# Optimization experiments

Measured on AMD Instinct MI355X. Metric: run time of the kernel, lower is better.

Reference implementation:

```python
import jax, jax.numpy as jnp
import numpy as np

N_NODES = 100000
N_FEAT = 512
HIDDEN = 256
N_CLASSES = 40
N_EDGES = 1600000
K = 10
ALPHA = 0.1


def setup_inputs() -> dict:
    key = jax.random.key(0)
    ks = jax.random.split(key, 8)
    feat = jax.random.normal(ks[0], (N_NODES, N_FEAT), dtype=jnp.float32)
    src = jax.random.randint(ks[1], (N_EDGES,), 0, N_NODES, dtype=jnp.int32)
    dst = jax.random.randint(ks[2], (N_EDGES,), 0, N_NODES, dtype=jnp.int32)
    # linear layers (PyTorch-style uniform init)
    s1 = 1.0 / np.sqrt(N_FEAT)
    W1 = jax.random.uniform(ks[3], (N_FEAT, HIDDEN), minval=-s1, maxval=s1, dtype=jnp.float32)
    b1 = jax.random.uniform(ks[4], (HIDDEN,), minval=-s1, maxval=s1, dtype=jnp.float32)
    s2 = 1.0 / np.sqrt(HIDDEN)
    W2 = jax.random.uniform(ks[5], (HIDDEN, N_CLASSES), minval=-s2, maxval=s2, dtype=jnp.float32)
    b2 = jax.random.uniform(ks[6], (N_CLASSES,), minval=-s2, maxval=s2, dtype=jnp.float32)
    # PPR init for per-hop weights: temp[k] = alpha*(1-alpha)^k, temp[K] = (1-alpha)^K
    temp = ALPHA * (1.0 - ALPHA) ** np.arange(K + 1)
    temp[-1] = (1.0 - ALPHA) ** K
    temp = jnp.asarray(temp, dtype=jnp.float32)
    return {"feat": feat, "W1": W1, "b1": b1, "W2": W2, "b2": b2,
            "temp": temp, "src": src, "dst": dst}


def reference(feat, W1, b1, W2, b2, temp, src, dst):
    N = feat.shape[0]
    # dgl.add_self_loop
    loop = jnp.arange(N, dtype=src.dtype)
    src_f = jnp.concatenate([src, loop])
    dst_f = jnp.concatenate([dst, loop])
    # MLP: lin1 -> relu -> lin2 (dropout is identity at inference)
    h = jax.nn.relu(feat @ W1 + b1) @ W2 + b2  # [N, C]
    # symmetric normalization: norm_e = d[dst] * d[src], d = deg^{-1/2}
    deg = jax.ops.segment_sum(jnp.ones_like(dst_f, dtype=h.dtype), dst_f, num_segments=N)
    d = jax.lax.rsqrt(deg)  # deg >= 1 due to self loops
    norm = (d[dst_f] * d[src_f])[:, None]  # [E, 1]
    # K-hop propagation with learned per-hop weights
    TH = h * temp[0]
    for k in range(K):
        msg = h[src_f] * norm                     # gather + edge scale
        h = jax.ops.segment_sum(msg, dst_f, num_segments=N)  # scatter-sum
        TH = TH + h * temp[k + 1]
    return jax.nn.log_softmax(TH, axis=1)
```

## Files before the change

kernel.cpp:

```cpp
#include <hip/hip_runtime.h>
#include <math.h>
#include <stdint.h>

#define N_NODES 100000
#define N_FEAT  512
#define HIDDEN  256
#define N_CLS   40
#define N_EDGES 1600000
#define K_HOPS  10

#define NPART   8
#define PSZ     12500
#define NPN     (NPART * N_NODES)
#define SCANB   782
#define HPAD    64

#define PB      51
#define PGRID   ((N_NODES + PB - 1) / PB)
#define ECAP    2048

typedef __attribute__((ext_vector_type(8))) short short8;
typedef __attribute__((ext_vector_type(4))) float f4_t;

__device__ __forceinline__ short f2bf(float f) {
    union { float f; unsigned u; } x; x.f = f;
    unsigned r = x.u + 0x7fffu + ((x.u >> 16) & 1u);
    return (short)(r >> 16);
}

__device__ __forceinline__ float bf2f(short b) {
    union { unsigned u; float f; } x;
    x.u = ((unsigned)(unsigned short)b) << 16;
    return x.f;
}

__device__ __forceinline__ unsigned cvtpk(float lo, float hi) {
    unsigned r;
    asm("v_cvt_pk_bf16_f32 %0, %1, %2" : "=v"(r) : "v"(lo), "v"(hi));
    return r;
}


__global__ __launch_bounds__(256) void init_degp_kernel(int* __restrict__ degp) {
    int idx = blockIdx.x * 256 + threadIdx.x;
    if (idx < NPN) {
        int v = idx >> 3, p = idx & 7;
        degp[idx] = (p == v / PSZ) ? 1 : 0;
    }
}

__global__ __launch_bounds__(256) void count_dst_kernel(const int* __restrict__ src,
                                                        const int* __restrict__ dst,
                                                        int* __restrict__ degp) {
    int e = blockIdx.x * 256 + threadIdx.x;
    if (e < N_EDGES) atomicAdd(&degp[dst[e] * NPART + src[e] / PSZ], 1);
}

__global__ __launch_bounds__(256) void rsqrt_deg_kernel(const int* __restrict__ degp,
                                                        float* __restrict__ d) {
    int v = blockIdx.x * 256 + threadIdx.x;
    if (v < N_NODES) {
        int s = 0;
#pragma unroll
        for (int p = 0; p < NPART; ++p) s += degp[v * NPART + p];
        d[v] = rsqrtf((float)s);
    }
}


__global__ __launch_bounds__(1024) void scan_partial_kernel(const int* __restrict__ degp,
                                                            int* __restrict__ blocksum) {
    __shared__ int s[1024];
    int t = threadIdx.x;
    int idx = blockIdx.x * 1024 + t;
    s[t] = (idx < NPN) ? degp[idx] : 0;
    __syncthreads();
#pragma unroll
    for (int off = 512; off > 0; off >>= 1) {
        if (t < off) s[t] += s[t + off];
        __syncthreads();
    }
    if (t == 0) blocksum[blockIdx.x] = s[0];
}

__global__ __launch_bounds__(1024) void scan_blocks_kernel(const int* __restrict__ blocksum,
                                                           int* __restrict__ blockoff) {
    __shared__ int s[1024];
    int t = threadIdx.x;
    int v = (t < SCANB) ? blocksum[t] : 0;
    s[t] = v;
    __syncthreads();
#pragma unroll
    for (int off = 1; off < 1024; off <<= 1) {
        int add = (t >= off) ? s[t - off] : 0;
        __syncthreads();
        s[t] += add;
        __syncthreads();
    }
    if (t < SCANB) blockoff[t] = s[t] - v;
}

__global__ __launch_bounds__(1024) void scan_write_kernel(const int* __restrict__ degp,
                                                          const int* __restrict__ blockoff,
                                                          int* __restrict__ rowptrp,
                                                          int* __restrict__ cursor) {
    __shared__ int s[1024];
    int t = threadIdx.x;
    int idx = blockIdx.x * 1024 + t;
    int v = (idx < NPN) ? degp[idx] : 0;
    s[t] = v;
    __syncthreads();
#pragma unroll
    for (int off = 1; off < 1024; off <<= 1) {
        int add = (t >= off) ? s[t - off] : 0;
        __syncthreads();
        s[t] += add;
        __syncthreads();
    }
    int pre = s[t] - v + blockoff[blockIdx.x];
    if (idx <= NPN) rowptrp[idx] = pre;
    if (idx < NPN) cursor[idx] = pre;
}

__global__ __launch_bounds__(256) void scatter_edges_kernel(const int* __restrict__ src,
                                                            const int* __restrict__ dst,
                                                            const float* __restrict__ d,
                                                            int* __restrict__ cursor,
                                                            int2* __restrict__ epair) {
    int e = blockIdx.x * 256 + threadIdx.x;
    if (e >= N_EDGES) return;
    int u = src[e], v = dst[e];
    int pos = atomicAdd(&cursor[v * NPART + u / PSZ], 1);
    int2 p;
    p.x = u * 128;
    p.y = __float_as_int(d[u] * d[v]);
    epair[pos] = p;
}

__global__ __launch_bounds__(256) void scatter_self_kernel(const float* __restrict__ d,
                                                           int* __restrict__ cursor,
                                                           int2* __restrict__ epair) {
    int v = blockIdx.x * 256 + threadIdx.x;
    if (v >= N_NODES) return;
    int pos = atomicAdd(&cursor[v * NPART + v / PSZ], 1);
    float dv = d[v];
    int2 p;
    p.x = v * 128;
    p.y = __float_as_int(dv * dv);
    epair[pos] = p;
}

__global__ __launch_bounds__(256) void cvt_w1_kernel(const float* __restrict__ W1,
                                                     short* __restrict__ W1T) {
    int lin = blockIdx.x * 256 + threadIdx.x;
    int k = lin >> 8, n = lin & 255;
    W1T[n * 512 + k] = f2bf(W1[lin]);
}

__global__ __launch_bounds__(256) void cvt_w2_kernel(const float* __restrict__ W2,
                                                     short* __restrict__ W2T) {
    int lin = blockIdx.x * 256 + threadIdx.x;
    int n = lin >> 8, k = lin & 255;
    W2T[lin] = (n < N_CLS) ? f2bf(W2[k * N_CLS + n]) : (short)0;
}

__global__ __launch_bounds__(256) void mlp_kernel(const float* __restrict__ feat,
                                                  const short* __restrict__ W1T,
                                                  const float* __restrict__ b1,
                                                  const short* __restrict__ W2T,
                                                  const float* __restrict__ b2,
                                                  const float* __restrict__ temp,
                                                  short* __restrict__ h,
                                                  float* __restrict__ TH) {
    __shared__ union {
        short A[2][64][72];
        short sH[64][264];
        struct { short Ho[64][40]; float To[64][40]; } o;
    } S;

    const int tid = threadIdx.x;
    const int rbase = blockIdx.x * 64;
    const int lane = tid & 63;
    const int wv = tid >> 6;
    const int quad = lane >> 4;
    const int l15 = lane & 15;

    f4_t acc[4][4];
#pragma unroll
    for (int m = 0; m < 4; ++m)
#pragma unroll
        for (int n = 0; n < 4; ++n) acc[m][n] = (f4_t)0.f;

    const int srow = tid >> 2;
    const int scol = (tid & 3) * 16;
    int growc = rbase + srow;
    if (growc >= N_NODES) growc = N_NODES - 1;
    const float* fp = feat + (size_t)growc * N_FEAT + scol;

    f4_t fR0, fR1, fR2, fR3;
    short8 bR[8];

#define LOADF(KT)                                                   \
    { const f4_t* p_ = (const f4_t*)(fp + (KT) * 64);               \
      fR0 = p_[0]; fR1 = p_[1]; fR2 = p_[2]; fR3 = p_[3]; }

#define LOADB(KT)                                                   \
    { const short* wb_ = W1T + (KT) * 64;                           \
      _Pragma("unroll")                                             \
      for (int kk2 = 0; kk2 < 2; ++kk2)                             \
          _Pragma("unroll")                                         \
          for (int n = 0; n < 4; ++n)                               \
              bR[kk2 * 4 + n] = *(const short8*)(                   \
                  wb_ + (wv * 64 + n * 16 + l15) * 512 + kk2 * 32 + quad * 8); }

#define CVTWR(BUF)                                                  \
    { union { unsigned u[4]; short8 s; } xlo_, xhi_;                \
      xlo_.u[0] = cvtpk(fR0[0], fR0[1]); xlo_.u[1] = cvtpk(fR0[2], fR0[3]); \
      xlo_.u[2] = cvtpk(fR1[0], fR1[1]); xlo_.u[3] = cvtpk(fR1[2], fR1[3]); \
      xhi_.u[0] = cvtpk(fR2[0], fR2[1]); xhi_.u[1] = cvtpk(fR2[2], fR2[3]); \
      xhi_.u[2] = cvtpk(fR3[0], fR3[1]); xhi_.u[3] = cvtpk(fR3[2], fR3[3]); \
      short8* dp_ = (short8*)&S.A[BUF][srow][scol];                 \
      dp_[0] = xlo_.s; dp_[1] = xhi_.s; }

#define BARRIER()                                                   \
    asm volatile("s_waitcnt lgkmcnt(0)" ::: "memory");              \
    __builtin_amdgcn_s_barrier();                                   \
    __builtin_amdgcn_sched_barrier(0);

    LOADF(0);
    LOADB(0);
    CVTWR(0);
    LOADF(1);
    BARRIER();

#pragma unroll
    for (int kt = 0; kt < 8; ++kt) {
        const int cb = kt & 1;
#pragma unroll
        for (int kk2 = 0; kk2 < 2; ++kk2) {
            short8 af[4];
#pragma unroll
            for (int m = 0; m < 4; ++m)
                af[m] = *(const short8*)&S.A[cb][m * 16 + l15][kk2 * 32 + quad * 8];
#pragma unroll
            for (int m = 0; m < 4; ++m)
#pragma unroll
                for (int n = 0; n < 4; ++n)
                    acc[m][n] = __builtin_amdgcn_mfma_f32_16x16x32_bf16(
                        af[m], bR[kk2 * 4 + n], acc[m][n], 0, 0, 0);
        }
        if (kt < 7) {
            LOADB(kt + 1);
            CVTWR(cb ^ 1);
        }
        if (kt < 6) LOADF(kt + 2);
        BARRIER();
    }
#undef LOADF
#undef LOADB
#undef CVTWR

#pragma unroll
    for (int n = 0; n < 4; ++n) {
        int col = wv * 64 + n * 16 + l15;
        float bb = b1[col];
#pragma unroll
        for (int m = 0; m < 4; ++m)
#pragma unroll
            for (int r = 0; r < 4; ++r) {
                float v = acc[m][n][r] + bb;
                S.sH[m * 16 + quad * 4 + r][col] = f2bf(v > 0.f ? v : 0.f);
            }
    }
    __syncthreads();

    f4_t accB[3];
#pragma unroll
    for (int n = 0; n < 3; ++n) accB[n] = (f4_t)0.f;
#pragma unroll
    for (int kk = 0; kk < 256; kk += 32) {
        short8 a = *(const short8*)&S.sH[wv * 16 + l15][kk + quad * 8];
#pragma unroll
        for (int n = 0; n < 3; ++n) {
            short8 b = *(const short8*)(W2T + (n * 16 + l15) * 256 + kk + quad * 8);
            accB[n] = __builtin_amdgcn_mfma_f32_16x16x32_bf16(a, b, accB[n], 0, 0, 0);
        }
    }
    __syncthreads();

    float t0 = temp[0];
#pragma unroll
    for (int n = 0; n < 3; ++n) {
        int col = n * 16 + l15;
        if (col < N_CLS) {
            float bb = b2[col];
#pragma unroll
            for (int r = 0; r < 4; ++r) {
                int row = wv * 16 + quad * 4 + r;
                float v = accB[n][r] + bb;
                S.o.Ho[row][col] = f2bf(v);
                S.o.To[row][col] = t0 * v;
            }
        }
    }
    __syncthreads();

    int rows = N_NODES - rbase; if (rows > 64) rows = 64;
    int nh = rows * 5;
    for (int i = tid; i < nh; i += 256) {
        int row = i / 5, part = i - row * 5;
        *(short8*)(h + (size_t)(rbase + row) * HPAD + part * 8) =
            *(const short8*)&S.o.Ho[row][part * 8];
    }
    int nt = rows * 10;
    for (int i = tid; i < nt; i += 256)
        *(f4_t*)(TH + (size_t)rbase * N_CLS + i * 4) =
            *(const f4_t*)((const float*)&S.o.To[0][0] + i * 4);
}

__global__ __launch_bounds__(256, 8) void prop_kernel(const short* __restrict__ h,
                                                      short* __restrict__ hn,
                                                      const int* __restrict__ rowptrp,
                                                      const int2* __restrict__ epair,
                                                      float* __restrict__ TH,
                                                      const float* __restrict__ temp,
                                                      int kidx) {
    __shared__ long long sE[ECAP];
    __shared__ int sRP[64];

    const int t = threadIdx.x;
    const int v0 = blockIdx.x * PB;
    int nmax = N_NODES - v0; if (nmax > PB) nmax = PB;
    if (t <= nmax) sRP[t] = rowptrp[(v0 + t) * NPART];
    __syncthreads();
    const int S0 = sRP[0];
    const int count = sRP[nmax] - S0;

    const int n = t / 5;
    const int c = t - n * 5;
    const bool act = (n < nmax) && (t < 255);
    const int js = act ? (sRP[n] - S0) : 0;
    const int je = act ? (sRP[n + 1] - S0) : 0;
    const char* hB = (const char*)h + c * 16;

    f4_t a0 = (f4_t)0.f, a1 = (f4_t)0.f;
    int j = js;
    for (int base = 0; base < count; base += ECAP) {
        int lim = count - base; if (lim > ECAP) lim = ECAP;
        __syncthreads();
        for (int i = t; i < lim; i += 256)
            sE[i] = *(const long long*)(epair + (size_t)(S0 + base + i));
        __syncthreads();
        int jend = je - base; if (jend > lim) jend = lim;
        int jj = j - base;
        for (; jj + 4 <= jend; jj += 4) {
            long long r0 = sE[jj], r1 = sE[jj + 1], r2 = sE[jj + 2], r3 = sE[jj + 3];
            short8 h0 = *(const short8*)(hB + (unsigned)(int)r0);
            short8 h1 = *(const short8*)(hB + (unsigned)(int)r1);
            short8 h2 = *(const short8*)(hB + (unsigned)(int)r2);
            short8 h3 = *(const short8*)(hB + (unsigned)(int)r3);
            float w0 = __int_as_float((int)(r0 >> 32));
            float w1 = __int_as_float((int)(r1 >> 32));
            float w2 = __int_as_float((int)(r2 >> 32));
            float w3 = __int_as_float((int)(r3 >> 32));
#pragma unroll
            for (int i = 0; i < 4; ++i) {
                a0[i] += w0 * bf2f(h0[i]) + w1 * bf2f(h1[i]) + w2 * bf2f(h2[i]) +
                         w3 * bf2f(h3[i]);
                a1[i] += w0 * bf2f(h0[4 + i]) + w1 * bf2f(h1[4 + i]) +
                         w2 * bf2f(h2[4 + i]) + w3 * bf2f(h3[4 + i]);
            }
        }
        for (; jj < jend; ++jj) {
            long long r = sE[jj];
            short8 hb8 = *(const short8*)(hB + (unsigned)(int)r);
            float w = __int_as_float((int)(r >> 32));
#pragma unroll
            for (int i = 0; i < 4; ++i) {
                a0[i] += w * bf2f(hb8[i]);
                a1[i] += w * bf2f(hb8[4 + i]);
            }
        }
        if (jend > 0 && j < base + jend) j = base + jend;
    }

    if (!act) return;
    int v = v0 + n;
    float tk = temp[kidx];
    short8 ob;
#pragma unroll
    for (int i = 0; i < 4; ++i) { ob[i] = f2bf(a0[i]); ob[4 + i] = f2bf(a1[i]); }
    *(short8*)(hn + (size_t)v * HPAD + c * 8) = ob;
    float* pt = TH + (size_t)v * N_CLS + c * 8;
    f4_t t0v = *(const f4_t*)pt;
    f4_t t1v = *(((const f4_t*)pt) + 1);
    t0v += tk * a0;
    t1v += tk * a1;
    *(f4_t*)pt = t0v;
    *(((f4_t*)pt) + 1) = t1v;
}

__global__ __launch_bounds__(256) void lsm_kernel(float* __restrict__ out) {
    int wid = (blockIdx.x * 256 + threadIdx.x) >> 6;
    int lane = threadIdx.x & 63;
    if (wid >= N_NODES) return;
    float x = (lane < N_CLS) ? out[wid * N_CLS + lane] : -INFINITY;
    float m = x;
#pragma unroll
    for (int o = 32; o > 0; o >>= 1) m = fmaxf(m, __shfl_xor(m, o, 64));
    float e = (lane < N_CLS) ? expf(x - m) : 0.f;
    float s = e;
#pragma unroll
    for (int o = 32; o > 0; o >>= 1) s += __shfl_xor(s, o, 64);
    float r = x - m - logf(s);
    if (lane < N_CLS) out[wid * N_CLS + lane] = r;
}


extern "C" void kernel_launch(void* const* d_in, const int* in_sizes, int n_in,
                              void* d_out, int out_size, void* d_ws, size_t ws_size,
                              hipStream_t stream) {
    const float* feat = (const float*)d_in[0];
    const float* W1   = (const float*)d_in[1];
    const float* b1   = (const float*)d_in[2];
    const float* W2   = (const float*)d_in[3];
    const float* b2   = (const float*)d_in[4];
    const float* temp = (const float*)d_in[5];
    const int*   src  = (const int*)d_in[6];
    const int*   dst  = (const int*)d_in[7];
    float* out = (float*)d_out;

    char* ws = (char*)d_ws;
    int*   degp    = (int*)(ws + 0);
    short* W1T     = (short*)(ws + 0);
    short* W2T     = (short*)(ws + 262144);
    float* dnorm   = (float*)(ws + 3200000);
    int*   rowptrp = (int*)(ws + 3600000);
    int*   cursor  = (int*)(ws + 6800016);
    int2*  epair   = (int2*)(ws + 10000016);
    short* h0      = (short*)(ws + 23600016);
    short* h1      = (short*)(ws + 36400016);
    int*   blocksum = (int*)(ws + 49200016);
    int*   blockoff = (int*)(ws + 49203152);

    init_degp_kernel<<<(NPN + 255) / 256, 256, 0, stream>>>(degp);
    count_dst_kernel<<<(N_EDGES + 255) / 256, 256, 0, stream>>>(src, dst, degp);
    rsqrt_deg_kernel<<<(N_NODES + 255) / 256, 256, 0, stream>>>(degp, dnorm);
    scan_partial_kernel<<<SCANB, 1024, 0, stream>>>(degp, blocksum);
    scan_blocks_kernel<<<1, 1024, 0, stream>>>(blocksum, blockoff);
    scan_write_kernel<<<SCANB, 1024, 0, stream>>>(degp, blockoff, rowptrp, cursor);
    cvt_w1_kernel<<<512, 256, 0, stream>>>(W1, W1T);
    cvt_w2_kernel<<<64, 256, 0, stream>>>(W2, W2T);
    scatter_edges_kernel<<<(N_EDGES + 255) / 256, 256, 0, stream>>>(src, dst, dnorm, cursor,
                                                                    epair);
    scatter_self_kernel<<<(N_NODES + 255) / 256, 256, 0, stream>>>(dnorm, cursor, epair);

    mlp_kernel<<<(N_NODES + 63) / 64, 256, 0, stream>>>(feat, W1T, b1, W2T, b2, temp, h0, out);

    short* hc = h0;
    short* hn = h1;
    for (int k = 0; k < K_HOPS; ++k) {
        prop_kernel<<<PGRID, 256, 0, stream>>>(hc, hn, rowptrp, epair, out, temp, k + 1);
        short* t = hc; hc = hn; hn = t;
    }

    lsm_kernel<<<(N_NODES / 4), 256, 0, stream>>>(out);
}
```

Baseline: 844.2 us.

## Balance propagation edges evenly across thread groups with shared-memory atomic accumulation

The propagation kernel now splits each block's edge chunk evenly across the 51 thread groups instead of giving each group one destination node's edges. A binary search over the row pointers tags each staged edge with its local destination, and per-group partial sums are flushed into a shared-memory accumulator with atomics whenever the destination changes. This targets load imbalance from uneven node degrees. In exchange it adds per-edge binary searches, shared atomics, a larger shared footprint, and a halved edge staging capacity, which means more chunk iterations.

```diff
diff --git a/kernel.cpp b/kernel.cpp
--- a/kernel.cpp
+++ b/kernel.cpp
@@ -17,7 +17,7 @@
 
 #define PB      51
 #define PGRID   ((N_NODES + PB - 1) / PB)
-#define ECAP    2048
+#define ECAP    1024
 
 typedef __attribute__((ext_vector_type(8))) short short8;
 typedef __attribute__((ext_vector_type(4))) float f4_t;
@@ -326,35 +326,66 @@
                                                       const float* __restrict__ temp,
                                                       int kidx) {
     __shared__ long long sE[ECAP];
+    __shared__ short sD[ECAP];
+    __shared__ float sAcc[PB * 40];
     __shared__ int sRP[64];
 
     const int t = threadIdx.x;
     const int v0 = blockIdx.x * PB;
     int nmax = N_NODES - v0; if (nmax > PB) nmax = PB;
     if (t <= nmax) sRP[t] = rowptrp[(v0 + t) * NPART];
+    for (int i = t; i < PB * 40; i += 256) sAcc[i] = 0.f;
     __syncthreads();
     const int S0 = sRP[0];
     const int count = sRP[nmax] - S0;
 
-    const int n = t / 5;
-    const int c = t - n * 5;
-    const bool act = (n < nmax) && (t < 255);
-    const int js = act ? (sRP[n] - S0) : 0;
-    const int je = act ? (sRP[n + 1] - S0) : 0;
+    const int g = t / 5;
+    const int c = t - g * 5;
     const char* hB = (const char*)h + c * 16;
 
     f4_t a0 = (f4_t)0.f, a1 = (f4_t)0.f;
-    int j = js;
+    int cur = -1;
+
+#define FLUSH()                                                     \
+    if (cur >= 0) {                                                 \
+        float* ap_ = &sAcc[cur * 40 + c * 8];                       \
+        _Pragma("unroll")                                           \
+        for (int i = 0; i < 4; ++i) {                               \
+            atomicAdd(ap_ + i, a0[i]);                              \
+            atomicAdd(ap_ + 4 + i, a1[i]);                          \
+        }                                                           \
+        a0 = (f4_t)0.f; a1 = (f4_t)0.f;                             \
+    }
+
+#define PROC(D, W, HV)                                              \
+    { int d_ = (D);                                                 \
+      if (d_ != cur) { FLUSH(); cur = d_; }                         \
+      float w_ = (W);                                               \
+      _Pragma("unroll")                                             \
+      for (int i = 0; i < 4; ++i) {                                 \
+          a0[i] += w_ * bf2f((HV)[i]);                              \
+          a1[i] += w_ * bf2f((HV)[4 + i]);                          \
+      } }
+
     for (int base = 0; base < count; base += ECAP) {
         int lim = count - base; if (lim > ECAP) lim = ECAP;
-        __syncthreads();
-        for (int i = t; i < lim; i += 256)
+        for (int i = t; i < lim; i += 256) {
             sE[i] = *(const long long*)(epair + (size_t)(S0 + base + i));
-        __syncthreads();
-        int jend = je - base; if (jend > lim) jend = lim;
-        int jj = j - base;
-        for (; jj + 4 <= jend; jj += 4) {
+            int gidx = S0 + base + i;
+            int lo = 0, hi2 = nmax;
+            while (hi2 - lo > 1) {
+                int mid = (lo + hi2) >> 1;
+                if (sRP[mid] <= gidx) lo = mid; else hi2 = mid;
+            }
+            sD[i] = (short)lo;
+        }
+        __syncthreads();
+        int lo_e = 0, hi_e = 0;
+        if (t < 255) { lo_e = (g * lim) / PB; hi_e = ((g + 1) * lim) / PB; }
+        int jj = lo_e;
+        for (; jj + 4 <= hi_e; jj += 4) {
             long long r0 = sE[jj], r1 = sE[jj + 1], r2 = sE[jj + 2], r3 = sE[jj + 3];
+            int d0 = sD[jj], d1 = sD[jj + 1], d2 = sD[jj + 2], d3 = sD[jj + 3];
             short8 h0 = *(const short8*)(hB + (unsigned)(int)r0);
             short8 h1 = *(const short8*)(hB + (unsigned)(int)r1);
             short8 h2 = *(const short8*)(hB + (unsigned)(int)r2);
@@ -363,41 +394,44 @@
             float w1 = __int_as_float((int)(r1 >> 32));
             float w2 = __int_as_float((int)(r2 >> 32));
             float w3 = __int_as_float((int)(r3 >> 32));
-#pragma unroll
-            for (int i = 0; i < 4; ++i) {
-                a0[i] += w0 * bf2f(h0[i]) + w1 * bf2f(h1[i]) + w2 * bf2f(h2[i]) +
-                         w3 * bf2f(h3[i]);
-                a1[i] += w0 * bf2f(h0[4 + i]) + w1 * bf2f(h1[4 + i]) +
-                         w2 * bf2f(h2[4 + i]) + w3 * bf2f(h3[4 + i]);
-            }
-        }
-        for (; jj < jend; ++jj) {
+            PROC(d0, w0, h0);
+            PROC(d1, w1, h1);
+            PROC(d2, w2, h2);
+            PROC(d3, w3, h3);
+        }
+        for (; jj < hi_e; ++jj) {
             long long r = sE[jj];
-            short8 hb8 = *(const short8*)(hB + (unsigned)(int)r);
+            int d = sD[jj];
+            short8 hv = *(const short8*)(hB + (unsigned)(int)r);
             float w = __int_as_float((int)(r >> 32));
-#pragma unroll
-            for (int i = 0; i < 4; ++i) {
-                a0[i] += w * bf2f(hb8[i]);
-                a1[i] += w * bf2f(hb8[4 + i]);
-            }
-        }
-        if (jend > 0 && j < base + jend) j = base + jend;
-    }
-
-    if (!act) return;
-    int v = v0 + n;
-    float tk = temp[kidx];
-    short8 ob;
-#pragma unroll
-    for (int i = 0; i < 4; ++i) { ob[i] = f2bf(a0[i]); ob[4 + i] = f2bf(a1[i]); }
-    *(short8*)(hn + (size_t)v * HPAD + c * 8) = ob;
-    float* pt = TH + (size_t)v * N_CLS + c * 8;
-    f4_t t0v = *(const f4_t*)pt;
-    f4_t t1v = *(((const f4_t*)pt) + 1);
-    t0v += tk * a0;
-    t1v += tk * a1;
-    *(f4_t*)pt = t0v;
-    *(((f4_t*)pt) + 1) = t1v;
+            PROC(d, w, hv);
+        }
+        FLUSH();
+        cur = -1;
+        __syncthreads();
+    }
+#undef PROC
+#undef FLUSH
+
+    if (t < 255 && g < nmax) {
+        int v = v0 + g;
+        float tk = temp[kidx];
+        const float* ap = &sAcc[g * 40 + c * 8];
+        f4_t r0v, r1v;
+#pragma unroll
+        for (int i = 0; i < 4; ++i) { r0v[i] = ap[i]; r1v[i] = ap[4 + i]; }
+        short8 ob;
+#pragma unroll
+        for (int i = 0; i < 4; ++i) { ob[i] = f2bf(r0v[i]); ob[4 + i] = f2bf(r1v[i]); }
+        *(short8*)(hn + (size_t)v * HPAD + c * 8) = ob;
+        float* pt = TH + (size_t)v * N_CLS + c * 8;
+        f4_t t0v = *(const f4_t*)pt;
+        f4_t t1v = *(((const f4_t*)pt) + 1);
+        t0v += tk * r0v;
+        t1v += tk * r1v;
+        *(f4_t*)pt = t0v;
+        *(((f4_t*)pt) + 1) = t1v;
+    }
 }
 
 __global__ __launch_bounds__(256) void lsm_kernel(float* __restrict__ out) {
```

Result: slower. 1.072 ms (+27.0%).
